# Performance work log

Measured on AMD Instinct MI355X. Metric: run time of the kernel, lower is better.

Reference implementation:

```python
import jax, jax.numpy as jnp
import numpy as np

NEAR, FAR = 2.0, 6.0
N_SAMPLES = 64
L_PTS, L_DIR = 10, 4
INF_DELTA = 1e10


def posenc(x, L):
    # x: [..., 3] -> [..., 3 + 6*L] (identity + sin/cos at 2^l frequencies)
    freqs = 2.0 ** jnp.arange(L, dtype=x.dtype)              # [L]
    ang = x[..., None, :] * freqs[:, None]                   # [..., L, 3]
    enc = jnp.concatenate([jnp.sin(ang), jnp.cos(ang)], axis=-1)  # [..., L, 6]
    return jnp.concatenate([x, enc.reshape(x.shape[:-1] + (L * 6,))], axis=-1)


def setup_inputs() -> dict:
    key = jax.random.key(0)
    ks = jax.random.split(key, 12)
    R, D, DH = 4096, 256, 128
    PE_P, PE_D = 3 + 6 * L_PTS, 3 + 6 * L_DIR  # 63, 27

    def w(k, shape):
        fan_in = shape[0]
        return jax.random.normal(k, shape, dtype=jnp.float32) / np.sqrt(fan_in)

    return {
        "xyz": jax.random.normal(ks[0], (1, R, 3), dtype=jnp.float32),
        "viewdirs": jax.random.normal(ks[1], (1, R, 3), dtype=jnp.float32),
        "W1": w(ks[2], (PE_P, D)), "b1": jnp.zeros((D,), jnp.float32),
        "W2": w(ks[3], (D, D)),    "b2": jnp.zeros((D,), jnp.float32),
        "W3": w(ks[4], (D, D)),    "b3": jnp.zeros((D,), jnp.float32),
        "Wsig": w(ks[5], (D, 1)),  "bsig": jnp.zeros((1,), jnp.float32),
        "Wfeat": w(ks[6], (D, D)), "bfeat": jnp.zeros((D,), jnp.float32),
        "Wdir": w(ks[7], (D + PE_D, DH)), "bdir": jnp.zeros((DH,), jnp.float32),
        "Wrgb": w(ks[8], (DH, 3)), "brgb": jnp.zeros((3,), jnp.float32),
    }


def reference(xyz, viewdirs, W1, b1, W2, b2, W3, b3, Wsig, bsig,
              Wfeat, bfeat, Wdir, bdir, Wrgb, brgb):
    xyz = xyz[0]          # [R, 3] (batch dim squeezed as in render_coarse)
    vd = viewdirs[0]
    vd = vd / jnp.linalg.norm(vd, axis=-1, keepdims=True)
    R = xyz.shape[0]

    # Evenly spaced samples between near and far (perturb=0 -> deterministic)
    t = jnp.linspace(0.0, 1.0, N_SAMPLES, dtype=xyz.dtype)
    samples = NEAR * (1.0 - t) + FAR * t                     # [N]
    samples = jnp.broadcast_to(samples, (R, N_SAMPLES))      # [R, N]
    delta = jnp.concatenate(
        [samples[:, 1:] - samples[:, :-1],
         jnp.full((R, 1), INF_DELTA, dtype=samples.dtype)], axis=-1)  # [R, N]

    # Sample points along each ray
    pts = xyz[:, None, :] + samples[..., None] * vd[:, None, :]  # [R, N, 3]

    # NeRF MLP: positional-encoded points -> density + view-dep color
    pe = posenc(pts, L_PTS)                                   # [R, N, 63]
    de = posenc(vd, L_DIR)                                    # [R, 27]
    h = jax.nn.relu(pe @ W1 + b1)
    h = jax.nn.relu(h @ W2 + b2)
    h = jax.nn.relu(h @ W3 + b3)                              # [R, N, 256]
    density = (h @ Wsig + bsig)[..., 0]                       # [R, N]
    feat = h @ Wfeat + bfeat                                  # [R, N, 256]
    de_b = jnp.broadcast_to(de[:, None, :], (R, N_SAMPLES, de.shape[-1]))
    hd = jax.nn.relu(jnp.concatenate([feat, de_b], axis=-1) @ Wdir + bdir)
    rgb = jax.nn.sigmoid(hd @ Wrgb + brgb)                    # [R, N, 3]

    # Volume rendering (alpha compositing with cumprod transmittance)
    sigma = jax.nn.relu(density)
    alpha = 1.0 - jnp.exp(-sigma * delta)                     # [R, N]
    T = jnp.concatenate(
        [jnp.ones((R, 1), alpha.dtype),
         jnp.cumprod(1.0 - alpha[:, :-1], axis=-1)], axis=-1)
    w = T * alpha                                             # [R, N]
    rgb_map = jnp.sum(w[..., None] * rgb, axis=-2)            # [R, 3]
    alpha_map = jnp.sum(w, axis=-1, keepdims=True)            # [R, 1]
    rgb_map = rgb_map + (1.0 - alpha_map)                     # white_bkgd
    depth_map = jnp.sum(w * samples, axis=-1)                 # [R]
    return rgb_map, depth_map, alpha_map
```

## Files before the change

kernel.cpp:

```cpp
#include <hip/hip_runtime.h>
#include <hip/hip_bf16.h>
#include <math.h>


typedef unsigned short u16;
typedef unsigned int   u32;
typedef _Float16 f16;
typedef _Float16 f16x8 __attribute__((ext_vector_type(8)));
typedef float    f32x4 __attribute__((ext_vector_type(4)));

#define ACT_STRIDE 296
#define NROW 64

__device__ __align__(16) f16 g_w[249856];

constexpr int OFF_W1 = 0;
constexpr int OFF_W2 = 16384;
constexpr int OFF_W3 = 81920;
constexpr int OFF_WF = 147456;
constexpr int OFF_WD = 212992;

static __device__ __forceinline__ float wash(float x) {
  return (x == x) ? x : 0.0f;
}

struct alignas(8) F16x4 { f16 x, y, z, w; };

__global__ void repack_kernel(const float* __restrict__ w1, const float* __restrict__ w2,
                              const float* __restrict__ w3, const float* __restrict__ wf,
                              const float* __restrict__ wd) {
  int e = blockIdx.x * 256 + threadIdx.x;
  const float* src; int K, N, ks, base;
  if (e < 81920)       { if (e < 16384) { src = w1; K = 63;  N = 256; ks = 2; base = OFF_W1; }
                         else           { src = w2; K = 256; N = 256; ks = 8; base = OFF_W2; } }
  else if (e < 147456) { src = w3; K = 256; N = 256; ks = 8; base = OFF_W3; }
  else if (e < 212992) { src = wf; K = 256; N = 256; ks = 8; base = OFF_WF; }
  else                 { src = wd; K = 283; N = 128; ks = 9; base = OFF_WD; }
  int le   = e - base;
  int f    = le >> 9, pos = le & 511;
  int lane = pos >> 3, j = pos & 7;
  int t    = f / ks,  s = f - t * ks;
  int k    = s * 32 + ((lane >> 4) << 3) + j;
  int n    = (t << 4) + (lane & 15);
  g_w[e] = (k < K) ? (f16)src[k * N + n] : (f16)0.0f;
}

template<int KS, int NT, int RT, bool RELU>
static __device__ __forceinline__ void mlp_layer(f16* act,
                                                 const f16* __restrict__ w_,
                                                 const float* __restrict__ bias,
                                                 int rg, int cg, int lane) {
  f32x4 acc[RT][NT];
#pragma unroll
  for (int rt = 0; rt < RT; ++rt)
#pragma unroll
    for (int nt = 0; nt < NT; ++nt) {
      f32x4 z = {0.0f, 0.0f, 0.0f, 0.0f};
      acc[rt][nt] = z;
    }
  const int l15 = lane & 15, q = lane >> 4;
#pragma unroll
  for (int s = 0; s < KS; ++s) {
    f16x8 af[RT];
#pragma unroll
    for (int rt = 0; rt < RT; ++rt) {
      const int row = (rg * RT + rt) * 16 + l15;
      af[rt] = *reinterpret_cast<const f16x8*>(&act[row * ACT_STRIDE + s * 32 + q * 8]);
    }
    f16x8 wf[NT];
#pragma unroll
    for (int nt = 0; nt < NT; ++nt) {
      const int t = cg * NT + nt;
      wf[nt] = *reinterpret_cast<const f16x8*>(&w_[(t * KS + s) * 512 + lane * 8]);
    }
#pragma unroll
    for (int rt = 0; rt < RT; ++rt)
#pragma unroll
      for (int nt = 0; nt < NT; ++nt)
        acc[rt][nt] = __builtin_amdgcn_mfma_f32_16x16x32_f16(
            wf[nt], af[rt], acc[rt][nt], 0, 0, 0);
  }
  __syncthreads();
#pragma unroll
  for (int nt = 0; nt < NT; ++nt) {
    const int nb = (cg * NT + nt) * 16 + q * 4;
    const float b0 = bias[nb + 0], b1 = bias[nb + 1];
    const float b2 = bias[nb + 2], b3 = bias[nb + 3];
#pragma unroll
    for (int rt = 0; rt < RT; ++rt) {
      const int row = (rg * RT + rt) * 16 + l15;
      float v0 = acc[rt][nt][0] + b0;
      float v1 = acc[rt][nt][1] + b1;
      float v2 = acc[rt][nt][2] + b2;
      float v3 = acc[rt][nt][3] + b3;
      if (RELU) {
        v0 = fmaxf(v0, 0.0f); v1 = fmaxf(v1, 0.0f);
        v2 = fmaxf(v2, 0.0f); v3 = fmaxf(v3, 0.0f);
      }
      F16x4 o; o.x = (f16)v0; o.y = (f16)v1; o.z = (f16)v2; o.w = (f16)v3;
      *reinterpret_cast<F16x4*>(&act[row * ACT_STRIDE + nb]) = o;
    }
  }
  __syncthreads();
}

__global__ __launch_bounds__(512, 4)
void nerf_kernel(const float* __restrict__ xyz, const float* __restrict__ vdirs,
                 const float* __restrict__ w1f, const float* __restrict__ b1,
                 const float* __restrict__ w2f, const float* __restrict__ b2,
                 const float* __restrict__ w3f, const float* __restrict__ b3,
                 const float* __restrict__ wsig, const float* __restrict__ bsig,
                 const float* __restrict__ bfeat, const float* __restrict__ bdir,
                 const float* __restrict__ wrgb, const float* __restrict__ brgb,
                 float* __restrict__ out) {
  __shared__ f16  s_act[NROW * ACT_STRIDE];
  __shared__ float s_geo[6];
  __shared__ float s_de[32];
  __shared__ float s_pe[64];
  __shared__ float s_h0[256], s_h1[256];
  __shared__ float s_sig;

  const int tid  = threadIdx.x;
  const int wave = tid >> 6;
  const int lane = tid & 63;
  const int rg   = wave >> 2;
  const int cg   = wave & 3;

  if (tid == 0) {
    int rgI = blockIdx.x;
    float vx = vdirs[rgI * 3 + 0];
    float vy = vdirs[rgI * 3 + 1];
    float vz = vdirs[rgI * 3 + 2];
    float inv = 1.0f / sqrtf(vx * vx + vy * vy + vz * vz + 1e-20f);
    s_geo[0] = xyz[rgI * 3 + 0];
    s_geo[1] = xyz[rgI * 3 + 1];
    s_geo[2] = xyz[rgI * 3 + 2];
    s_geo[3] = vx * inv;
    s_geo[4] = vy * inv;
    s_geo[5] = vz * inv;
  }
  __syncthreads();

  if (tid < 32) {
    float val = 0.0f;
    if (tid < 3) val = s_geo[3 + tid];
    else if (tid < 27) {
      int fi = tid - 3, l = fi / 6, m = fi % 6;
      int ii = (m < 3) ? m : m - 3;
      float ang = s_geo[3 + ii] * (float)(1 << l);
      val = (m < 3) ? sinf(ang) : cosf(ang);
    }
    s_de[tid] = val;
  }

  if (tid >= 64 && tid < 128) {
    int f = tid - 64;
    float p[3];
    p[0] = s_geo[0] + 6.0f * s_geo[3];
    p[1] = s_geo[1] + 6.0f * s_geo[4];
    p[2] = s_geo[2] + 6.0f * s_geo[5];
    float val = 0.0f;
    if (f < 3) val = p[f];
    else if (f < 63) {
      int fi = f - 3, l = fi / 6, m = fi % 6;
      int ii = (m < 3) ? m : m - 3;
      float ang = p[ii] * (float)(1 << l);
      val = (m < 3) ? sinf(ang) : cosf(ang);
    }
    s_pe[f] = val;
  }

  {
    int row = tid >> 3, c8 = tid & 7;
    float t  = (float)row * (1.0f / 63.0f);
    float ts = 2.0f * (1.0f - t) + 6.0f * t;
    float p[3];
    p[0] = s_geo[0] + ts * s_geo[3];
    p[1] = s_geo[1] + ts * s_geo[4];
    p[2] = s_geo[2] + ts * s_geo[5];
#pragma unroll
    for (int j = 0; j < 8; ++j) {
      int f = c8 * 8 + j;
      float val;
      if (f < 3) val = p[f];
      else if (f == 63) val = 0.0f;
      else {
        int fi = f - 3, l = fi / 6, m = fi % 6;
        int ii = (m < 3) ? m : m - 3;
        float ang = p[ii] * (float)(1 << l);
        val = (m < 3) ? sinf(ang) : cosf(ang);
      }
      s_act[row * ACT_STRIDE + f] = (f16)val;
    }
  }
  __syncthreads();

  if (tid < 256) {
    float a = b1[tid];
    for (int k = 0; k < 63; ++k) a = fmaf(w1f[k * 256 + tid], s_pe[k], a);
    s_h0[tid] = fmaxf(a, 0.0f);
  }
  __syncthreads();
  if (tid < 256) {
    float a = b2[tid];
#pragma unroll 4
    for (int k = 0; k < 256; ++k) a = fmaf(w2f[k * 256 + tid], s_h0[k], a);
    s_h1[tid] = fmaxf(a, 0.0f);
  }
  __syncthreads();
  if (tid < 256) {
    float a = b3[tid];
#pragma unroll 4
    for (int k = 0; k < 256; ++k) a = fmaf(w3f[k * 256 + tid], s_h1[k], a);
    s_h0[tid] = fmaxf(a, 0.0f);
  }
  __syncthreads();
  if (tid < 64) {
    float a = s_h0[tid * 4 + 0] * wsig[tid * 4 + 0]
            + s_h0[tid * 4 + 1] * wsig[tid * 4 + 1]
            + s_h0[tid * 4 + 2] * wsig[tid * 4 + 2]
            + s_h0[tid * 4 + 3] * wsig[tid * 4 + 3];
#pragma unroll
    for (int o = 32; o > 0; o >>= 1) a += __shfl_xor(a, o, 64);
    if (tid == 0) s_sig = wash(a + bsig[0]);
  }

  mlp_layer<2, 4, 2, true>(s_act, g_w + OFF_W1, b1, rg, cg, lane);
  mlp_layer<8, 4, 2, true>(s_act, g_w + OFF_W2, b2, rg, cg, lane);
  mlp_layer<8, 4, 2, true>(s_act, g_w + OFF_W3, b3, rg, cg, lane);

  float my_den = 0.0f;
  if (tid < 64) {
    float a = 0.0f;
    const float4* wp = reinterpret_cast<const float4*>(wsig);
#pragma unroll 8
    for (int k4 = 0; k4 < 64; ++k4) {
      F16x4 h = *reinterpret_cast<const F16x4*>(&s_act[tid * ACT_STRIDE + k4 * 4]);
      float4 w = wp[k4];
      a += (float)h.x * w.x + (float)h.y * w.y + (float)h.z * w.z + (float)h.w * w.w;
    }
    my_den = wash(a + bsig[0]);
  }

  mlp_layer<8, 4, 2, false>(s_act, g_w + OFF_WF, bfeat, rg, cg, lane);

  {
    int row = tid >> 3, i0 = (tid & 7) * 4;
#pragma unroll
    for (int j = 0; j < 4; ++j)
      s_act[row * ACT_STRIDE + 256 + i0 + j] = (f16)s_de[i0 + j];
  }
  __syncthreads();

  mlp_layer<9, 2, 2, true>(s_act, g_w + OFF_WD, bdir, rg, cg, lane);

  float r0 = 0.0f, r1 = 0.0f, r2 = 0.0f;
  if (tid < 64) {
    float a0 = brgb[0], a1 = brgb[1], a2 = brgb[2];
#pragma unroll 8
    for (int k = 0; k < 128; ++k) {
      float hv = (float)s_act[tid * ACT_STRIDE + k];
      a0 += hv * wrgb[k * 3 + 0];
      a1 += hv * wrgb[k * 3 + 1];
      a2 += hv * wrgb[k * 3 + 2];
    }
    a0 = wash(a0); a1 = wash(a1); a2 = wash(a2);
    r0 = 1.0f / (1.0f + expf(-a0));
    r1 = 1.0f / (1.0f + expf(-a1));
    r2 = 1.0f / (1.0f + expf(-a2));
  }

  if (wave == 0) {
    int rgI = blockIdx.x;
    float t  = (float)lane * (1.0f / 63.0f);
    float ts = 2.0f * (1.0f - t) + 6.0f * t;
    float delta;
    if (lane < 63) {
      float t2 = (float)(lane + 1) * (1.0f / 63.0f);
      delta = (2.0f * (1.0f - t2) + 6.0f * t2) - ts;
    } else delta = 1e10f;
    float den = (lane == 63) ? s_sig : my_den;
    float sig = fmaxf(den, 0.0f);
    float sd  = fminf(sig * delta, 60.0f);
    float incl = sd;
#pragma unroll
    for (int o = 1; o < 64; o <<= 1) {
      float v = __shfl_up(incl, o, 64);
      if (lane >= o) incl += v;
    }
    float excl  = fminf(fmaxf(incl - sd, 0.0f), 60.0f);
    float T     = expf(-excl);
    float alpha = 1.0f - expf(-sd);
    float w     = T * alpha;
    float sw = w, swr = w * r0, swg = w * r1, swb = w * r2, swd = w * ts;
#pragma unroll
    for (int o = 32; o > 0; o >>= 1) {
      sw  += __shfl_xor(sw,  o, 64);
      swr += __shfl_xor(swr, o, 64);
      swg += __shfl_xor(swg, o, 64);
      swb += __shfl_xor(swb, o, 64);
      swd += __shfl_xor(swd, o, 64);
    }
    if (lane == 0) {
      float bg = 1.0f - sw;
      out[rgI * 3 + 0]  = swr + bg;
      out[rgI * 3 + 1]  = swg + bg;
      out[rgI * 3 + 2]  = swb + bg;
      out[12288 + rgI]  = swd;
      out[16384 + rgI]  = sw;
    }
  }
}

extern "C" void kernel_launch(void* const* d_in, const int* in_sizes, int n_in,
                              void* d_out, int out_size, void* d_ws, size_t ws_size,
                              hipStream_t stream) {
  const float* xyz   = (const float*)d_in[0];
  const float* vdirs = (const float*)d_in[1];
  const float* W1    = (const float*)d_in[2];
  const float* b1    = (const float*)d_in[3];
  const float* W2    = (const float*)d_in[4];
  const float* b2    = (const float*)d_in[5];
  const float* W3    = (const float*)d_in[6];
  const float* b3    = (const float*)d_in[7];
  const float* Wsig  = (const float*)d_in[8];
  const float* bsig  = (const float*)d_in[9];
  const float* Wfeat = (const float*)d_in[10];
  const float* bfeat = (const float*)d_in[11];
  const float* Wdir  = (const float*)d_in[12];
  const float* bdir  = (const float*)d_in[13];
  const float* Wrgb  = (const float*)d_in[14];
  const float* brgb  = (const float*)d_in[15];
  float* out = (float*)d_out;

  repack_kernel<<<dim3(976), dim3(256), 0, stream>>>(W1, W2, W3, Wfeat, Wdir);
  nerf_kernel<<<dim3(4096), dim3(512), 0, stream>>>(
      xyz, vdirs, W1, b1, W2, b2, W3, b3, Wsig, bsig, bfeat, bdir, Wrgb, brgb, out);
}
```

Baseline: 404.8 us.

## Process two rays per block and make the fp32 last-sample recompute conditional

Each block now handles two rays (128 sample rows) instead of one, halving the grid and doubling the MFMA row tiles per weight load, which improves weight reuse. The fp32 scalar recompute of the last sample's density (a full 3-layer matvec) now runs only when the f16 density at sample 63 is close to zero, by an ad hoc threshold. The last sample's huge delta makes its sign critical, and the fp32 path is kept only where the f16 result could have the wrong sign. The threshold is a heuristic tied to the f16 error magnitude and may not hold for all inputs. Shared memory per block grows, which may reduce occupancy.

```diff
diff --git a/kernel.cpp b/kernel.cpp
--- a/kernel.cpp
+++ b/kernel.cpp
@@ -10,7 +10,8 @@
 typedef float    f32x4 __attribute__((ext_vector_type(4)));
 
 #define ACT_STRIDE 296
-#define NROW 64
+#define NROW 128
+#define EPS_D63 0.25f
 
 __device__ __align__(16) f16 g_w[249856];
 
@@ -114,11 +115,12 @@
                  const float* __restrict__ wrgb, const float* __restrict__ brgb,
                  float* __restrict__ out) {
   __shared__ f16  s_act[NROW * ACT_STRIDE];
-  __shared__ float s_geo[6];
-  __shared__ float s_de[32];
+  __shared__ float s_geo[2][6];
+  __shared__ float s_de[2][32];
+  __shared__ float s_den63[2];
+  __shared__ float s_sig[2];
   __shared__ float s_pe[64];
   __shared__ float s_h0[256], s_h1[256];
-  __shared__ float s_sig;
 
   const int tid  = threadIdx.x;
   const int wave = tid >> 6;
@@ -126,61 +128,46 @@
   const int rg   = wave >> 2;
   const int cg   = wave & 3;
 
-  if (tid == 0) {
-    int rgI = blockIdx.x;
-    float vx = vdirs[rgI * 3 + 0];
-    float vy = vdirs[rgI * 3 + 1];
-    float vz = vdirs[rgI * 3 + 2];
+  if (tid < 2) {
+    int r = blockIdx.x * 2 + tid;
+    float vx = vdirs[r * 3 + 0];
+    float vy = vdirs[r * 3 + 1];
+    float vz = vdirs[r * 3 + 2];
     float inv = 1.0f / sqrtf(vx * vx + vy * vy + vz * vz + 1e-20f);
-    s_geo[0] = xyz[rgI * 3 + 0];
-    s_geo[1] = xyz[rgI * 3 + 1];
-    s_geo[2] = xyz[rgI * 3 + 2];
-    s_geo[3] = vx * inv;
-    s_geo[4] = vy * inv;
-    s_geo[5] = vz * inv;
-  }
-  __syncthreads();
-
-  if (tid < 32) {
+    s_geo[tid][0] = xyz[r * 3 + 0];
+    s_geo[tid][1] = xyz[r * 3 + 1];
+    s_geo[tid][2] = xyz[r * 3 + 2];
+    s_geo[tid][3] = vx * inv;
+    s_geo[tid][4] = vy * inv;
+    s_geo[tid][5] = vz * inv;
+  }
+  __syncthreads();
+
+  if (tid < 64) {
+    int ray = tid >> 5, i = tid & 31;
     float val = 0.0f;
-    if (tid < 3) val = s_geo[3 + tid];
-    else if (tid < 27) {
-      int fi = tid - 3, l = fi / 6, m = fi % 6;
+    if (i < 3) val = s_geo[ray][3 + i];
+    else if (i < 27) {
+      int fi = i - 3, l = fi / 6, m = fi % 6;
       int ii = (m < 3) ? m : m - 3;
-      float ang = s_geo[3 + ii] * (float)(1 << l);
+      float ang = s_geo[ray][3 + ii] * (float)(1 << l);
       val = (m < 3) ? sinf(ang) : cosf(ang);
     }
-    s_de[tid] = val;
-  }
-
-  if (tid >= 64 && tid < 128) {
-    int f = tid - 64;
-    float p[3];
-    p[0] = s_geo[0] + 6.0f * s_geo[3];
-    p[1] = s_geo[1] + 6.0f * s_geo[4];
-    p[2] = s_geo[2] + 6.0f * s_geo[5];
-    float val = 0.0f;
-    if (f < 3) val = p[f];
-    else if (f < 63) {
-      int fi = f - 3, l = fi / 6, m = fi % 6;
-      int ii = (m < 3) ? m : m - 3;
-      float ang = p[ii] * (float)(1 << l);
-      val = (m < 3) ? sinf(ang) : cosf(ang);
-    }
-    s_pe[f] = val;
+    s_de[ray][i] = val;
   }
 
   {
-    int row = tid >> 3, c8 = tid & 7;
-    float t  = (float)row * (1.0f / 63.0f);
+    int row = tid >> 2, q4 = tid & 3;
+    int ray = row >> 6, n = row & 63;
+    float t  = (float)n * (1.0f / 63.0f);
     float ts = 2.0f * (1.0f - t) + 6.0f * t;
     float p[3];
-    p[0] = s_geo[0] + ts * s_geo[3];
-    p[1] = s_geo[1] + ts * s_geo[4];
-    p[2] = s_geo[2] + ts * s_geo[5];
-#pragma unroll
-    for (int j = 0; j < 8; ++j) {
-      int f = c8 * 8 + j;
+    p[0] = s_geo[ray][0] + ts * s_geo[ray][3];
+    p[1] = s_geo[ray][1] + ts * s_geo[ray][4];
+    p[2] = s_geo[ray][2] + ts * s_geo[ray][5];
+#pragma unroll 4
+    for (int f0 = 0; f0 < 16; ++f0) {
+      int f = q4 * 16 + f0;
       float val;
       if (f < 3) val = p[f];
       else if (f == 63) val = 0.0f;
@@ -195,42 +182,12 @@
   }
   __syncthreads();
 
-  if (tid < 256) {
-    float a = b1[tid];
-    for (int k = 0; k < 63; ++k) a = fmaf(w1f[k * 256 + tid], s_pe[k], a);
-    s_h0[tid] = fmaxf(a, 0.0f);
-  }
-  __syncthreads();
-  if (tid < 256) {
-    float a = b2[tid];
-#pragma unroll 4
-    for (int k = 0; k < 256; ++k) a = fmaf(w2f[k * 256 + tid], s_h0[k], a);
-    s_h1[tid] = fmaxf(a, 0.0f);
-  }
-  __syncthreads();
-  if (tid < 256) {
-    float a = b3[tid];
-#pragma unroll 4
-    for (int k = 0; k < 256; ++k) a = fmaf(w3f[k * 256 + tid], s_h1[k], a);
-    s_h0[tid] = fmaxf(a, 0.0f);
-  }
-  __syncthreads();
-  if (tid < 64) {
-    float a = s_h0[tid * 4 + 0] * wsig[tid * 4 + 0]
-            + s_h0[tid * 4 + 1] * wsig[tid * 4 + 1]
-            + s_h0[tid * 4 + 2] * wsig[tid * 4 + 2]
-            + s_h0[tid * 4 + 3] * wsig[tid * 4 + 3];
-#pragma unroll
-    for (int o = 32; o > 0; o >>= 1) a += __shfl_xor(a, o, 64);
-    if (tid == 0) s_sig = wash(a + bsig[0]);
-  }
-
-  mlp_layer<2, 4, 2, true>(s_act, g_w + OFF_W1, b1, rg, cg, lane);
-  mlp_layer<8, 4, 2, true>(s_act, g_w + OFF_W2, b2, rg, cg, lane);
-  mlp_layer<8, 4, 2, true>(s_act, g_w + OFF_W3, b3, rg, cg, lane);
+  mlp_layer<2, 4, 4, true>(s_act, g_w + OFF_W1, b1, rg, cg, lane);
+  mlp_layer<8, 4, 4, true>(s_act, g_w + OFF_W2, b2, rg, cg, lane);
+  mlp_layer<8, 4, 4, true>(s_act, g_w + OFF_W3, b3, rg, cg, lane);
 
   float my_den = 0.0f;
-  if (tid < 64) {
+  if (tid < 128) {
     float a = 0.0f;
     const float4* wp = reinterpret_cast<const float4*>(wsig);
 #pragma unroll 8
@@ -240,22 +197,25 @@
       a += (float)h.x * w.x + (float)h.y * w.y + (float)h.z * w.z + (float)h.w * w.w;
     }
     my_den = wash(a + bsig[0]);
-  }
-
-  mlp_layer<8, 4, 2, false>(s_act, g_w + OFF_WF, bfeat, rg, cg, lane);
+    if (tid == 63)  s_den63[0] = my_den;
+    if (tid == 127) s_den63[1] = my_den;
+  }
+
+  mlp_layer<8, 4, 4, false>(s_act, g_w + OFF_WF, bfeat, rg, cg, lane);
 
   {
-    int row = tid >> 3, i0 = (tid & 7) * 4;
-#pragma unroll
-    for (int j = 0; j < 4; ++j)
-      s_act[row * ACT_STRIDE + 256 + i0 + j] = (f16)s_de[i0 + j];
-  }
-  __syncthreads();
-
-  mlp_layer<9, 2, 2, true>(s_act, g_w + OFF_WD, bdir, rg, cg, lane);
+    int row = tid >> 2, i0 = (tid & 3) * 8;
+    int ray = row >> 6;
+#pragma unroll
+    for (int j = 0; j < 8; ++j)
+      s_act[row * ACT_STRIDE + 256 + i0 + j] = (f16)s_de[ray][i0 + j];
+  }
+  __syncthreads();
+
+  mlp_layer<9, 2, 4, true>(s_act, g_w + OFF_WD, bdir, rg, cg, lane);
 
   float r0 = 0.0f, r1 = 0.0f, r2 = 0.0f;
-  if (tid < 64) {
+  if (tid < 128) {
     float a0 = brgb[0], a1 = brgb[1], a2 = brgb[2];
 #pragma unroll 8
     for (int k = 0; k < 128; ++k) {
@@ -270,8 +230,61 @@
     r2 = 1.0f / (1.0f + expf(-a2));
   }
 
-  if (wave == 0) {
-    int rgI = blockIdx.x;
+#pragma unroll 1
+  for (int rr = 0; rr < 2; ++rr) {
+    if (fabsf(s_den63[rr]) < EPS_D63) {
+      if (tid < 64) {
+        float p[3];
+        p[0] = s_geo[rr][0] + 6.0f * s_geo[rr][3];
+        p[1] = s_geo[rr][1] + 6.0f * s_geo[rr][4];
+        p[2] = s_geo[rr][2] + 6.0f * s_geo[rr][5];
+        float val = 0.0f;
+        if (tid < 3) val = p[tid];
+        else if (tid < 63) {
+          int fi = tid - 3, l = fi / 6, m = fi % 6;
+          int ii = (m < 3) ? m : m - 3;
+          float ang = p[ii] * (float)(1 << l);
+          val = (m < 3) ? sinf(ang) : cosf(ang);
+        }
+        s_pe[tid] = val;
+      }
+      __syncthreads();
+      if (tid < 256) {
+        float a = b1[tid];
+        for (int k = 0; k < 63; ++k) a = fmaf(w1f[k * 256 + tid], s_pe[k], a);
+        s_h0[tid] = fmaxf(a, 0.0f);
+      }
+      __syncthreads();
+      if (tid < 256) {
+        float a = b2[tid];
+#pragma unroll 4
+        for (int k = 0; k < 256; ++k) a = fmaf(w2f[k * 256 + tid], s_h0[k], a);
+        s_h1[tid] = fmaxf(a, 0.0f);
+      }
+      __syncthreads();
+      if (tid < 256) {
+        float a = b3[tid];
+#pragma unroll 4
+        for (int k = 0; k < 256; ++k) a = fmaf(w3f[k * 256 + tid], s_h1[k], a);
+        s_h0[tid] = fmaxf(a, 0.0f);
+      }
+      __syncthreads();
+      if (tid < 64) {
+        float a = s_h0[tid * 4 + 0] * wsig[tid * 4 + 0]
+                + s_h0[tid * 4 + 1] * wsig[tid * 4 + 1]
+                + s_h0[tid * 4 + 2] * wsig[tid * 4 + 2]
+                + s_h0[tid * 4 + 3] * wsig[tid * 4 + 3];
+#pragma unroll
+        for (int o = 32; o > 0; o >>= 1) a += __shfl_xor(a, o, 64);
+        if (tid == 0) s_sig[rr] = wash(a + bsig[0]);
+      }
+      __syncthreads();
+    }
+  }
+  __syncthreads();
+
+  if (wave < 2) {
+    int r = blockIdx.x * 2 + wave;
     float t  = (float)lane * (1.0f / 63.0f);
     float ts = 2.0f * (1.0f - t) + 6.0f * t;
     float delta;
@@ -279,7 +292,8 @@
       float t2 = (float)(lane + 1) * (1.0f / 63.0f);
       delta = (2.0f * (1.0f - t2) + 6.0f * t2) - ts;
     } else delta = 1e10f;
-    float den = (lane == 63) ? s_sig : my_den;
+    float den = my_den;
+    if (lane == 63 && fabsf(s_den63[wave]) < EPS_D63) den = s_sig[wave];
     float sig = fmaxf(den, 0.0f);
     float sd  = fminf(sig * delta, 60.0f);
     float incl = sd;
@@ -303,11 +317,11 @@
     }
     if (lane == 0) {
       float bg = 1.0f - sw;
-      out[rgI * 3 + 0]  = swr + bg;
-      out[rgI * 3 + 1]  = swg + bg;
-      out[rgI * 3 + 2]  = swb + bg;
-      out[12288 + rgI]  = swd;
-      out[16384 + rgI]  = sw;
+      out[r * 3 + 0]  = swr + bg;
+      out[r * 3 + 1]  = swg + bg;
+      out[r * 3 + 2]  = swb + bg;
+      out[12288 + r]  = swd;
+      out[16384 + r]  = sw;
     }
   }
 }
@@ -334,6 +348,6 @@
   float* out = (float*)d_out;
 
   repack_kernel<<<dim3(976), dim3(256), 0, stream>>>(W1, W2, W3, Wfeat, Wdir);
-  nerf_kernel<<<dim3(4096), dim3(512), 0, stream>>>(
+  nerf_kernel<<<dim3(2048), dim3(512), 0, stream>>>(
       xyz, vdirs, W1, b1, W2, b2, W3, b3, Wsig, bsig, bfeat, bdir, Wrgb, brgb, out);
 }
```

After: 756.3 us. 1.87x slower.
